# Performance work log

Measured on AMD Instinct MI355X. Metric: run time of the kernel, lower is better.

Reference implementation:

```python
import jax, jax.numpy as jnp
import numpy as np
import math

DIM = 4096
N_HEADS = 32
N_KV_HEADS = 8
HEAD_DIM = DIM // N_HEADS  # 128
N_REP = N_HEADS // N_KV_HEADS  # 4
BATCH = 1
SEQ = 2048
ROPE_THETA = 10000.0


def setup_inputs() -> dict:
    key = jax.random.key(0)
    ks = jax.random.split(key, 6)
    x = jax.random.normal(ks[0], (BATCH, SEQ, DIM), dtype=jnp.float32)
    # torch nn.Linear weights are [out_features, in_features]
    s = 1.0 / math.sqrt(DIM)
    wq = jax.random.normal(ks[1], (N_HEADS * HEAD_DIM, DIM), dtype=jnp.float32) * s
    wk = jax.random.normal(ks[2], (N_KV_HEADS * HEAD_DIM, DIM), dtype=jnp.float32) * s
    wv = jax.random.normal(ks[3], (N_KV_HEADS * HEAD_DIM, DIM), dtype=jnp.float32) * s
    wo = jax.random.normal(ks[4], (DIM, N_HEADS * HEAD_DIM), dtype=jnp.float32) * s
    # precomputed rotary frequencies (real/imag parts of freqs_cis)
    inv_freq = 1.0 / (ROPE_THETA ** (jnp.arange(0, HEAD_DIM, 2, dtype=jnp.float32) / HEAD_DIM))
    t = jnp.arange(SEQ, dtype=jnp.float32)
    freqs = jnp.outer(t, inv_freq)  # [S, HEAD_DIM//2]
    return {"x": x, "wq": wq, "wk": wk, "wv": wv, "wo": wo,
            "freqs_cos": jnp.cos(freqs), "freqs_sin": jnp.sin(freqs)}


def _apply_rotary(t, cos, sin):
    # t: [B, S, H, HD]; cos/sin: [S, HD//2]
    B, S, H, HD = t.shape
    tr = t.reshape(B, S, H, HD // 2, 2)
    re, im = tr[..., 0], tr[..., 1]
    c = cos[None, :, None, :]
    s = sin[None, :, None, :]
    out_re = re * c - im * s
    out_im = re * s + im * c
    return jnp.stack([out_re, out_im], axis=-1).reshape(B, S, H, HD)


def reference(x, wq, wk, wv, wo, freqs_cos, freqs_sin):
    B, S, _ = x.shape
    q = jnp.einsum('bsd,od->bso', x, wq).reshape(B, S, N_HEADS, HEAD_DIM)
    k = jnp.einsum('bsd,od->bso', x, wk).reshape(B, S, N_KV_HEADS, HEAD_DIM)
    v = jnp.einsum('bsd,od->bso', x, wv).reshape(B, S, N_KV_HEADS, HEAD_DIM)
    q = _apply_rotary(q, freqs_cos, freqs_sin)
    k = _apply_rotary(k, freqs_cos, freqs_sin)
    # repeat kv heads (GQA): [B,S,Hkv,HD] -> [B,S,H,HD]
    k = jnp.repeat(k, N_REP, axis=2)
    v = jnp.repeat(v, N_REP, axis=2)
    # SDPA with causal mask
    scale = 1.0 / math.sqrt(HEAD_DIM)
    scores = jnp.einsum('bqhd,bkhd->bhqk', q, k) * scale
    causal = jnp.tril(jnp.ones((S, S), dtype=bool))
    scores = jnp.where(causal[None, None], scores, jnp.finfo(scores.dtype).min)
    attn = jax.nn.softmax(scores, axis=-1)
    y = jnp.einsum('bhqk,bkhd->bqhd', attn, v).reshape(B, S, N_HEADS * HEAD_DIM)
    return jnp.einsum('bso,do->bsd', y, wo)
```

## Files before the change

kernel.cpp:

```cpp
#include <hip/hip_runtime.h>
#include <hip/hip_bf16.h>
#include <stdint.h>

typedef unsigned short u16;
typedef __bf16 bf16_8 __attribute__((ext_vector_type(8)));
typedef float f32x4 __attribute__((ext_vector_type(4)));

#define SEQ 2048
#define DIM 4096
#define NH 32
#define NKV 8
#define HD 128
#define QSCALE 0.08838834764831845f

__device__ inline u16 f2bf(float f) {
    unsigned int u = __float_as_uint(f);
    unsigned int r = (u + 0x7fffu + ((u >> 16) & 1u)) >> 16;
    return (u16)r;
}

__device__ inline void async16(const void* g, void* l) {
    __builtin_amdgcn_global_load_lds(
        (const __attribute__((address_space(1))) void*)g,
        (__attribute__((address_space(3))) void*)l, 16, 0, 0);
}

__global__ __launch_bounds__(256) void cast_f32_bf16(const float* __restrict__ in,
                                                     u16* __restrict__ out, int n4) {
    int i = blockIdx.x * 256 + threadIdx.x;
    if (i >= n4) return;
    float4 v = ((const float4*)in)[i];
    ushort4 o;
    o.x = f2bf(v.x); o.y = f2bf(v.y); o.z = f2bf(v.z); o.w = f2bf(v.w);
    ((ushort4*)out)[i] = o;
}

template <int MODE>
__global__ __launch_bounds__(256) void gemm_bt(const u16* __restrict__ A,
                                               const u16* __restrict__ B,
                                               void* __restrict__ C0,
                                               void* __restrict__ C1,
                                               void* __restrict__ C2,
                                               const float* __restrict__ fc,
                                               const float* __restrict__ fs,
                                               int M, int N, int K) {
    __shared__ u16 As[128 * 32];
    __shared__ u16 Bs[128 * 32];
    const int tid = threadIdx.x;
    const int lane = tid & 63;
    const int wid = tid >> 6;
    const int quad = lane >> 4;
    const int l16 = lane & 15;
    const int wm = (wid >> 1) * 64;
    const int wn = (wid & 1) * 64;
    const int bm = blockIdx.y * 128;
    const int bn = blockIdx.x * 128;

    f32x4 acc[4][4] = {};

    for (int k0 = 0; k0 < K; k0 += 32) {
#pragma unroll
        for (int r = 0; r < 2; ++r) {
            int S = r * 256 + tid;
            int row = S >> 2;
            int slot = S & 3;
            int chunk = slot ^ ((row >> 1) & 3);
            const char* ga = (const char*)A + ((size_t)(bm + row) * K + k0 + chunk * 8) * 2;
            async16(ga, (char*)As + S * 16);
            const char* gb = (const char*)B + ((size_t)(bn + row) * K + k0 + chunk * 8) * 2;
            async16(gb, (char*)Bs + S * 16);
        }
        __syncthreads();
        const int cs = quad ^ ((l16 >> 1) & 3);
        bf16_8 a[4], b[4];
#pragma unroll
        for (int i = 0; i < 4; ++i)
            a[i] = *(const bf16_8*)&As[(wm + i * 16 + l16) * 32 + cs * 8];
#pragma unroll
        for (int j = 0; j < 4; ++j)
            b[j] = *(const bf16_8*)&Bs[(wn + j * 16 + l16) * 32 + cs * 8];
#pragma unroll
        for (int i = 0; i < 4; ++i)
#pragma unroll
            for (int j = 0; j < 4; ++j)
                acc[i][j] = __builtin_amdgcn_mfma_f32_16x16x32_bf16(a[i], b[j], acc[i][j], 0, 0, 0);
        __syncthreads();
    }

    if (MODE == 0) {
        float* Cf = (float*)C0;
#pragma unroll
        for (int i = 0; i < 4; ++i)
#pragma unroll
            for (int j = 0; j < 4; ++j)
#pragma unroll
                for (int r = 0; r < 4; ++r)
                    Cf[(size_t)(bm + wm + i * 16 + quad * 4 + r) * N + (bn + wn + j * 16 + l16)] =
                        acc[i][j][r];
    } else {
        u16* Qb = (u16*)C0;
        u16* Kb = (u16*)C1;
        u16* Vt = (u16*)C2;
        if (bn < 5120) {
            const bool isQ = bn < 4096;
            const float osc = isQ ? QSCALE : 1.0f;
#pragma unroll
            for (int i = 0; i < 4; ++i)
#pragma unroll
                for (int j = 0; j < 4; ++j) {
                    int n = bn + wn + j * 16 + l16;
                    int p = (n & 127) >> 1;
                    bool odd = (l16 & 1);
#pragma unroll
                    for (int r = 0; r < 4; ++r) {
                        int m = bm + wm + i * 16 + quad * 4 + r;
                        float v = acc[i][j][r];
                        float u = __shfl_xor(v, 1);
                        float c = fc[m * 64 + p];
                        float s = fs[m * 64 + p];
                        float o = (odd ? (u * s + v * c) : (v * c - u * s)) * osc;
                        if (isQ)
                            Qb[(size_t)m * 4096 + n] = f2bf(o);
                        else
                            Kb[(size_t)m * 1024 + (n - 4096)] = f2bf(o);
                    }
                }
        } else {
#pragma unroll
            for (int i = 0; i < 4; ++i)
#pragma unroll
                for (int j = 0; j < 4; ++j) {
                    int n = bn + wn + j * 16 + l16;
                    ushort4 o;
                    o.x = f2bf(acc[i][j][0]);
                    o.y = f2bf(acc[i][j][1]);
                    o.z = f2bf(acc[i][j][2]);
                    o.w = f2bf(acc[i][j][3]);
                    *(ushort4*)&Vt[(size_t)(n - 5120) * SEQ + (bm + wm + i * 16 + quad * 4)] = o;
                }
        }
    }
}

__global__ __launch_bounds__(256, 4) void attn_k(const u16* __restrict__ Q,
                                                 const u16* __restrict__ Kb,
                                                 const u16* __restrict__ Vt,
                                                 u16* __restrict__ Y) {
    __shared__ u16 Ks[64 * 128];
    __shared__ u16 Vs[128 * 64];
    __shared__ u16 Ps[4 * 16 * 64];
    const int tid = threadIdx.x;
    const int lane = tid & 63;
    const int w = tid >> 6;
    const int quad = lane >> 4;
    const int l16 = lane & 15;
    const int id = blockIdx.x;
    const int qt = 31 - (id >> 5);
    const int h = id & 31;
    const int kvh = h >> 2;
    const size_t qrow0 = (size_t)qt * 64;

    bf16_8 qf[4];
#pragma unroll
    for (int ks = 0; ks < 4; ++ks)
        qf[ks] = *(const bf16_8*)&Q[(qrow0 + w * 16 + l16) * DIM + h * HD + ks * 32 + quad * 8];

    f32x4 po[8] = {};
    float l_r[4] = {0.f, 0.f, 0.f, 0.f};

    for (int kt = 0; kt <= qt; ++kt) {
#pragma unroll
        for (int r = 0; r < 4; ++r) {
            int S = r * 256 + tid;
            {
                int row = S >> 4, slot = S & 15;
                int chunk = slot ^ (row & 15);
                const char* g = (const char*)Kb +
                    (((size_t)kt * 64 + row) * 1024 + kvh * HD + chunk * 8) * 2;
                async16(g, (char*)Ks + S * 16);
            }
            {
                int row = S >> 3, slot = S & 7;
                int chunk = slot ^ (row & 7);
                const char* g = (const char*)Vt +
                    (((size_t)(kvh * HD + row)) * SEQ + kt * 64 + chunk * 8) * 2;
                async16(g, (char*)Vs + S * 16);
            }
        }
        __syncthreads();

        f32x4 sc[4] = {};
#pragma unroll
        for (int ks = 0; ks < 4; ++ks)
#pragma unroll
            for (int j = 0; j < 4; ++j) {
                bf16_8 kb = *(const bf16_8*)&Ks[(j * 16 + l16) * 128 + ((ks * 4 + quad) ^ l16) * 8];
                sc[j] = __builtin_amdgcn_mfma_f32_16x16x32_bf16(qf[ks], kb, sc[j], 0, 0, 0);
            }

        float pv[4][4];
#pragma unroll
        for (int j = 0; j < 4; ++j)
#pragma unroll
            for (int r = 0; r < 4; ++r)
                pv[j][r] = __expf(sc[j][r]);

        if (kt == qt) {
#pragma unroll
            for (int j = 0; j < 4; ++j) {
                int coli = j * 16 + l16;
#pragma unroll
                for (int r = 0; r < 4; ++r) {
                    int rowi = w * 16 + quad * 4 + r;
                    if (coli > rowi) pv[j][r] = 0.f;
                }
            }
        }

#pragma unroll
        for (int r = 0; r < 4; ++r) {
            l_r[r] += (pv[0][r] + pv[1][r]) + (pv[2][r] + pv[3][r]);
            int Rp = quad * 4 + r;
#pragma unroll
            for (int j = 0; j < 4; ++j) {
                int chunk = j * 2 + (l16 >> 3);
                int colp = ((chunk ^ (Rp & 7)) << 3) | (l16 & 7);
                Ps[w * 1024 + Rp * 64 + colp] = f2bf(pv[j][r]);
            }
        }

#pragma unroll
        for (int ks = 0; ks < 2; ++ks) {
            bf16_8 pf = *(const bf16_8*)&Ps[w * 1024 + l16 * 64 + (((ks * 4 + quad) ^ (l16 & 7))) * 8];
#pragma unroll
            for (int n = 0; n < 8; ++n) {
                bf16_8 vf = *(const bf16_8*)&Vs[(n * 16 + l16) * 64 + (((ks * 4 + quad) ^ (l16 & 7))) * 8];
                po[n] = __builtin_amdgcn_mfma_f32_16x16x32_bf16(pf, vf, po[n], 0, 0, 0);
            }
        }
        __syncthreads();
    }

#pragma unroll
    for (int r = 0; r < 4; ++r) {
        float l = l_r[r];
        l += __shfl_xor(l, 1);
        l += __shfl_xor(l, 2);
        l += __shfl_xor(l, 4);
        l += __shfl_xor(l, 8);
        float inv = 1.f / l;
        size_t row = qrow0 + w * 16 + quad * 4 + r;
#pragma unroll
        for (int n = 0; n < 8; ++n)
            Y[row * DIM + h * HD + n * 16 + l16] = f2bf(po[n][r] * inv);
    }
}

extern "C" void kernel_launch(void* const* d_in, const int* in_sizes, int n_in,
                              void* d_out, int out_size, void* d_ws, size_t ws_size,
                              hipStream_t stream) {
    const float* x  = (const float*)d_in[0];
    const float* wq = (const float*)d_in[1];
    const float* wk = (const float*)d_in[2];
    const float* wv = (const float*)d_in[3];
    const float* wo = (const float*)d_in[4];
    const float* fc = (const float*)d_in[5];
    const float* fs = (const float*)d_in[6];

    char* ws = (char*)d_ws;
    const size_t MB = 1u << 20;
    u16* xb    = (u16*)(ws);
    u16* wqkvb = (u16*)(ws + 16 * MB);
    u16* wob   = (u16*)(ws + 64 * MB);
    u16* Qb    = (u16*)(ws + 96 * MB);
    u16* Kb    = (u16*)(ws + 112 * MB);
    u16* Vtb   = (u16*)(ws + 116 * MB);
    u16* Yb    = (u16*)(ws + 120 * MB);

    cast_f32_bf16<<<(2048 * 4096 / 4) / 256, 256, 0, stream>>>(x, xb, 2048 * 4096 / 4);
    cast_f32_bf16<<<(4096 * 4096 / 4) / 256, 256, 0, stream>>>(wq, wqkvb, 4096 * 4096 / 4);
    cast_f32_bf16<<<(1024 * 4096 / 4) / 256, 256, 0, stream>>>(wk, wqkvb + (size_t)4096 * 4096, 1024 * 4096 / 4);
    cast_f32_bf16<<<(1024 * 4096 / 4) / 256, 256, 0, stream>>>(wv, wqkvb + (size_t)5120 * 4096, 1024 * 4096 / 4);
    cast_f32_bf16<<<(4096 * 4096 / 4) / 256, 256, 0, stream>>>(wo, wob, 4096 * 4096 / 4);

    gemm_bt<1><<<dim3(48, 16), 256, 0, stream>>>(xb, wqkvb, Qb, Kb, Vtb, fc, fs, 2048, 6144, 4096);

    attn_k<<<dim3(1024), 256, 0, stream>>>(Qb, Kb, Vtb, Yb);

    gemm_bt<0><<<dim3(32, 16), 256, 0, stream>>>(Yb, wob, (float*)d_out, nullptr, nullptr,
                                                 nullptr, nullptr, 2048, 4096, 4096);
}
```

Baseline: 539.4 us.

## Merge cast kernels, fold log2e into Q scale, transpose score MFMA

The five f32-to-bf16 cast launches become a single kernel that picks its source by element offset, which removes launch overhead. The Q scale now includes log2(e), so the attention kernel can use exp2f instead of __expf. The QK MFMA operands are swapped so each lane holds one query row's scores. This lets P be written to LDS as packed 8-byte stores and the row sum be reduced with fewer shuffles. The contiguous workspace layout matches the cast kernel's single destination, but it depends on the offsets xb=0, wqkvb=16MB and wob=64MB lining up exactly.

```diff
diff --git a/kernel.cpp b/kernel.cpp
--- a/kernel.cpp
+++ b/kernel.cpp
@@ -11,7 +11,7 @@
 #define NH 32
 #define NKV 8
 #define HD 128
-#define QSCALE 0.08838834764831845f
+#define QSCALE_LOG2E 0.12753785222167917f
 
 __device__ inline u16 f2bf(float f) {
     unsigned int u = __float_as_uint(f);
@@ -25,14 +25,25 @@
         (__attribute__((address_space(3))) void*)l, 16, 0, 0);
 }
 
-__global__ __launch_bounds__(256) void cast_f32_bf16(const float* __restrict__ in,
-                                                     u16* __restrict__ out, int n4) {
-    int i = blockIdx.x * 256 + threadIdx.x;
-    if (i >= n4) return;
-    float4 v = ((const float4*)in)[i];
+__global__ __launch_bounds__(256) void cast_all(const float* __restrict__ x,
+                                                const float* __restrict__ wq,
+                                                const float* __restrict__ wk,
+                                                const float* __restrict__ wv,
+                                                const float* __restrict__ wo,
+                                                u16* __restrict__ dst) {
+    size_t i4 = (size_t)blockIdx.x * 256 + threadIdx.x;
+    size_t e = i4 * 4;
+    const float* src;
+    size_t off;
+    if (e < 8388608ull)       { src = x;  off = 0; }
+    else if (e < 25165824ull) { src = wq; off = 8388608ull; }
+    else if (e < 29360128ull) { src = wk; off = 25165824ull; }
+    else if (e < 33554432ull) { src = wv; off = 29360128ull; }
+    else                      { src = wo; off = 33554432ull; }
+    float4 v = ((const float4*)src)[i4 - off / 4];
     ushort4 o;
     o.x = f2bf(v.x); o.y = f2bf(v.y); o.z = f2bf(v.z); o.w = f2bf(v.w);
-    ((ushort4*)out)[i] = o;
+    ((ushort4*)dst)[i4] = o;
 }
 
 template <int MODE>
@@ -103,7 +114,7 @@
         u16* Vt = (u16*)C2;
         if (bn < 5120) {
             const bool isQ = bn < 4096;
-            const float osc = isQ ? QSCALE : 1.0f;
+            const float osc = isQ ? QSCALE_LOG2E : 1.0f;
 #pragma unroll
             for (int i = 0; i < 4; ++i)
 #pragma unroll
@@ -166,7 +177,10 @@
         qf[ks] = *(const bf16_8*)&Q[(qrow0 + w * 16 + l16) * DIM + h * HD + ks * 32 + quad * 8];
 
     f32x4 po[8] = {};
-    float l_r[4] = {0.f, 0.f, 0.f, 0.f};
+    float lsum = 0.f;
+
+    char* psbase = (char*)Ps + w * 2048 + l16 * 128;
+    const int sw = (l16 & 7) << 1;
 
     for (int kt = 0; kt <= qt; ++kt) {
 #pragma unroll
@@ -193,45 +207,43 @@
 #pragma unroll
         for (int ks = 0; ks < 4; ++ks)
 #pragma unroll
-            for (int j = 0; j < 4; ++j) {
-                bf16_8 kb = *(const bf16_8*)&Ks[(j * 16 + l16) * 128 + ((ks * 4 + quad) ^ l16) * 8];
-                sc[j] = __builtin_amdgcn_mfma_f32_16x16x32_bf16(qf[ks], kb, sc[j], 0, 0, 0);
+            for (int jb = 0; jb < 4; ++jb) {
+                bf16_8 kb = *(const bf16_8*)&Ks[(jb * 16 + l16) * 128 + ((ks * 4 + quad) ^ l16) * 8];
+                sc[jb] = __builtin_amdgcn_mfma_f32_16x16x32_bf16(kb, qf[ks], sc[jb], 0, 0, 0);
             }
 
         float pv[4][4];
 #pragma unroll
-        for (int j = 0; j < 4; ++j)
+        for (int jb = 0; jb < 4; ++jb)
 #pragma unroll
             for (int r = 0; r < 4; ++r)
-                pv[j][r] = __expf(sc[j][r]);
+                pv[jb][r] = exp2f(sc[jb][r]);
 
         if (kt == qt) {
-#pragma unroll
-            for (int j = 0; j < 4; ++j) {
-                int coli = j * 16 + l16;
-#pragma unroll
-                for (int r = 0; r < 4; ++r) {
-                    int rowi = w * 16 + quad * 4 + r;
-                    if (coli > rowi) pv[j][r] = 0.f;
-                }
-            }
-        }
-
-#pragma unroll
-        for (int r = 0; r < 4; ++r) {
-            l_r[r] += (pv[0][r] + pv[1][r]) + (pv[2][r] + pv[3][r]);
-            int Rp = quad * 4 + r;
-#pragma unroll
-            for (int j = 0; j < 4; ++j) {
-                int chunk = j * 2 + (l16 >> 3);
-                int colp = ((chunk ^ (Rp & 7)) << 3) | (l16 & 7);
-                Ps[w * 1024 + Rp * 64 + colp] = f2bf(pv[j][r]);
-            }
+            int qloc = w * 16 + l16;
+#pragma unroll
+            for (int jb = 0; jb < 4; ++jb)
+#pragma unroll
+                for (int r = 0; r < 4; ++r)
+                    if (jb * 16 + quad * 4 + r > qloc) pv[jb][r] = 0.f;
+        }
+
+#pragma unroll
+        for (int jb = 0; jb < 4; ++jb) {
+            lsum += (pv[jb][0] + pv[jb][1]) + (pv[jb][2] + pv[jb][3]);
+            ushort4 pk;
+            pk.x = f2bf(pv[jb][0]);
+            pk.y = f2bf(pv[jb][1]);
+            pk.z = f2bf(pv[jb][2]);
+            pk.w = f2bf(pv[jb][3]);
+            int c = jb * 4 + quad;
+            *(ushort4*)(psbase + ((c ^ sw) << 3)) = pk;
         }
 
 #pragma unroll
         for (int ks = 0; ks < 2; ++ks) {
-            bf16_8 pf = *(const bf16_8*)&Ps[w * 1024 + l16 * 64 + (((ks * 4 + quad) ^ (l16 & 7))) * 8];
+            int c = ks * 8 + quad * 2;
+            bf16_8 pf = *(const bf16_8*)(psbase + ((c ^ sw) << 3));
 #pragma unroll
             for (int n = 0; n < 8; ++n) {
                 bf16_8 vf = *(const bf16_8*)&Vs[(n * 16 + l16) * 64 + (((ks * 4 + quad) ^ (l16 & 7))) * 8];
@@ -241,18 +253,16 @@
         __syncthreads();
     }
 
+    lsum += __shfl_xor(lsum, 16);
+    lsum += __shfl_xor(lsum, 32);
+    float inv = 1.f / lsum;
 #pragma unroll
     for (int r = 0; r < 4; ++r) {
-        float l = l_r[r];
-        l += __shfl_xor(l, 1);
-        l += __shfl_xor(l, 2);
-        l += __shfl_xor(l, 4);
-        l += __shfl_xor(l, 8);
-        float inv = 1.f / l;
+        float invr = __shfl(inv, quad * 4 + r);
         size_t row = qrow0 + w * 16 + quad * 4 + r;
 #pragma unroll
         for (int n = 0; n < 8; ++n)
-            Y[row * DIM + h * HD + n * 16 + l16] = f2bf(po[n][r] * inv);
+            Y[row * DIM + h * HD + n * 16 + l16] = f2bf(po[n][r] * invr);
     }
 }
 
@@ -277,11 +287,7 @@
     u16* Vtb   = (u16*)(ws + 116 * MB);
     u16* Yb    = (u16*)(ws + 120 * MB);
 
-    cast_f32_bf16<<<(2048 * 4096 / 4) / 256, 256, 0, stream>>>(x, xb, 2048 * 4096 / 4);
-    cast_f32_bf16<<<(4096 * 4096 / 4) / 256, 256, 0, stream>>>(wq, wqkvb, 4096 * 4096 / 4);
-    cast_f32_bf16<<<(1024 * 4096 / 4) / 256, 256, 0, stream>>>(wk, wqkvb + (size_t)4096 * 4096, 1024 * 4096 / 4);
-    cast_f32_bf16<<<(1024 * 4096 / 4) / 256, 256, 0, stream>>>(wv, wqkvb + (size_t)5120 * 4096, 1024 * 4096 / 4);
-    cast_f32_bf16<<<(4096 * 4096 / 4) / 256, 256, 0, stream>>>(wo, wob, 4096 * 4096 / 4);
+    cast_all<<<49152, 256, 0, stream>>>(x, wq, wk, wv, wo, (u16*)ws);
 
     gemm_bt<1><<<dim3(48, 16), 256, 0, stream>>>(xb, wqkvb, Qb, Kb, Vtb, fc, fs, 2048, 6144, 4096);
 
```

New measurement: 517.7 us. -4.0%, faster.
